# Kernel optimization log

Hardware: AMD Instinct MI355X
Metric: run time of the kernel (lower is better)

The kernel has to match this reference:

```python
import jax, jax.numpy as jnp
import numpy as np

N_HEAD = 16
HEAD_DIM = 64
N_EMBD = N_HEAD * HEAD_DIM
KS, STRIDE = 4, 4
LN_EPS = 1e-5


def _layernorm(x, g, b):
    mu = jnp.mean(x, axis=-1, keepdims=True)
    var = jnp.var(x, axis=-1, keepdims=True)
    return (x - mu) * jax.lax.rsqrt(var + LN_EPS) * g + b


def _depthwise_conv(x_bcl, w):
    # x_bcl: [N, head_dim, L], w: [head_dim, 1, KS] (torch Conv1d groups=head_dim layout)
    return jax.lax.conv_general_dilated(
        x_bcl, w, window_strides=(STRIDE,), padding='VALID',
        dimension_numbers=('NCH', 'OIH', 'NCH'), feature_group_count=HEAD_DIM)


def setup_inputs() -> dict:
    key = jax.random.key(0)
    ks = jax.random.split(key, 12)
    B, T, L = 8, 64, 4096
    s = 0.02
    return {
        'x': jax.random.normal(ks[0], (B, T, N_EMBD), jnp.float32),
        'cached_k': jax.random.normal(ks[1], (B, N_HEAD, L, HEAD_DIM), jnp.float32),
        'cached_v': jax.random.normal(ks[2], (B, N_HEAD, L, HEAD_DIM), jnp.float32),
        'w_attn': jax.random.normal(ks[3], (N_EMBD, 3 * N_EMBD), jnp.float32) * s,
        'b_attn': jnp.zeros((3 * N_EMBD,), jnp.float32),
        'w_proj': jax.random.normal(ks[4], (N_EMBD, N_EMBD), jnp.float32) * s,
        'b_proj': jnp.zeros((N_EMBD,), jnp.float32),
        'k_conv': jax.random.normal(ks[5], (HEAD_DIM, 1, KS), jnp.float32) * 0.5,
        'v_conv': jax.random.normal(ks[6], (HEAD_DIM, 1, KS), jnp.float32) * 0.5,
        'ln_k_g': jnp.ones((HEAD_DIM,), jnp.float32),
        'ln_k_b': jnp.zeros((HEAD_DIM,), jnp.float32),
        'ln_v_g': jnp.ones((HEAD_DIM,), jnp.float32),
        'ln_v_b': jnp.zeros((HEAD_DIM,), jnp.float32),
    }


def reference(x, cached_k, cached_v, w_attn, b_attn, w_proj, b_proj,
              k_conv, v_conv, ln_k_g, ln_k_b, ln_v_g, ln_v_b):
    B, T, C = x.shape
    H, hd = N_HEAD, HEAD_DIM
    qkv = x @ w_attn + b_attn                      # [B,T,3C]
    q, k, v = jnp.split(qkv, 3, axis=-1)
    q = q.reshape(B, T, H, hd).transpose(0, 2, 1, 3)  # [B,H,T,hd]
    k = k.reshape(B, T, H, hd).transpose(0, 2, 1, 3)
    v = v.reshape(B, T, H, hd).transpose(0, 2, 1, 3)

    # compress cached K/V: depthwise conv over cache length, then LayerNorm
    L = cached_k.shape[2]
    pk = cached_k.transpose(0, 1, 3, 2).reshape(B * H, hd, L)
    pv = cached_v.transpose(0, 1, 3, 2).reshape(B * H, hd, L)
    ck = _depthwise_conv(pk, k_conv).reshape(B, H, hd, -1).transpose(0, 1, 3, 2)  # [B,H,Lc,hd]
    cv = _depthwise_conv(pv, v_conv).reshape(B, H, hd, -1).transpose(0, 1, 3, 2)
    ck = jax.lax.stop_gradient(_layernorm(ck, ln_k_g, ln_k_b))
    cv = jax.lax.stop_gradient(_layernorm(cv, ln_v_g, ln_v_b))

    k_full = jnp.concatenate([ck, k], axis=2)      # [B,H,Tk,hd]
    v_full = jnp.concatenate([cv, v], axis=2)
    Tk = k_full.shape[2]

    # faithful to original: rectangular tril(T, Tk) -> query i sees keys j<=i
    mask = jnp.tril(jnp.ones((T, Tk), dtype=bool))
    att = jnp.einsum('bhqd,bhkd->bhqk', q, k_full) * (1.0 / np.sqrt(hd))
    att = jnp.where(mask[None, None], att, -jnp.inf)
    att = jax.nn.softmax(att, axis=-1)
    y = jnp.einsum('bhqk,bhkd->bhqd', att, v_full)
    y = y.transpose(0, 2, 1, 3).reshape(B, T, C)
    return y @ w_proj + b_proj
```

## Files before the change

### kernel.cpp

```cpp
#include <hip/hip_runtime.h>
#include <hip/hip_bf16.h>
#include <math.h>

#define NH 16
#define LCACHE 4096

typedef __attribute__((ext_vector_type(8))) short short8;
typedef __attribute__((ext_vector_type(8))) unsigned short ushort8;
typedef __attribute__((ext_vector_type(4))) float f32x4;

__device__ __forceinline__ unsigned short f2bf(float f) {
    __hip_bfloat16 b = __float2bfloat16(f);
    unsigned short u;
    __builtin_memcpy(&u, &b, 2);
    return u;
}

__global__ __launch_bounds__(256, 4)
void prep_kernel(const float* __restrict__ cached_k, const float* __restrict__ cached_v,
                 const float* __restrict__ kcw, const float* __restrict__ vcw,
                 const float* __restrict__ lkg, const float* __restrict__ lkb,
                 const float* __restrict__ lvg, const float* __restrict__ lvb,
                 const float* __restrict__ x, const float* __restrict__ w_attn,
                 const float* __restrict__ w_proj,
                 ushort* __restrict__ ckf, ushort* __restrict__ cvtf,
                 ushort* __restrict__ xp, ushort* __restrict__ wq,
                 ushort* __restrict__ wp)
{
    __shared__ float Wt[32][65];
    const int bid = blockIdx.x, tid = threadIdx.x;
    const int w = tid >> 6, l = tid & 63;

    const int bh = bid >> 3, sub = bid & 7;
    const int T = sub >> 2, quarter = sub & 3;
    const float* S = (T ? cached_v : cached_k) + (size_t)bh * (LCACHE * 64);
    float tap[4][4];
#pragma unroll
    for (int q = 0; q < 4; ++q) {
        int key = quarter * 16 + w * 4 + q;
        const float* p = S + (size_t)key * 256 + l;
        tap[q][0] = p[0]; tap[q][1] = p[64]; tap[q][2] = p[128]; tap[q][3] = p[192];
    }

    const int isP = bid >> 9;
    const int rem = bid & 511;
    const int ntw = rem >> 5, ktw = (rem >> 1) & 15, kbh = rem & 1;
    const float* W = isP ? w_proj : w_attn;
    const int ldw  = isP ? 1024 : 3072;
    ushort* D      = isP ? wp : wq;
    float wreg[8];
#pragma unroll
    for (int rep = 0; rep < 8; ++rep) {
        int lin = rep * 256 + tid;
        int kr = lin >> 6, nn = lin & 63;
        wreg[rep] = W[(size_t)(ktw * 64 + kbh * 32 + kr) * ldw + ntw * 64 + nn];
    }

    const int doX = (w == (bid & 3));
    float xr[8];
    if (doX) {
        int f = bid;
        int mt = f >> 6, kt = (f >> 2) & 15, fi = f & 3;
        int kb = fi >> 1, mb = fi & 1;
        int r = l & 15, kg8 = l >> 4;
        int m  = mt * 32 + mb * 16 + r;
        int k0 = kt * 64 + kb * 32 + kg8 * 8;
        const float* s = x + (size_t)m * 1024 + k0;
#pragma unroll
        for (int j = 0; j < 8; ++j) xr[j] = s[j];
    }

    {
        const float* cwp = T ? vcw : kcw;
        float4 w4v = *(const float4*)(cwp + l * 4);
        float g = (T ? lvg : lkg)[l], bb = (T ? lvb : lkb)[l];
        ushort* dstf = (T ? cvtf : ckf) + (size_t)bh * 4096;
        float av[4], s1[4], s2[4];
#pragma unroll
        for (int q = 0; q < 4; ++q) {
            float a = tap[q][0] * w4v.x;
            a = fmaf(tap[q][1], w4v.y, a);
            a = fmaf(tap[q][2], w4v.z, a);
            a = fmaf(tap[q][3], w4v.w, a);
            av[q] = a; s1[q] = a; s2[q] = a * a;
        }
#pragma unroll
        for (int o = 32; o; o >>= 1) {
#pragma unroll
            for (int q = 0; q < 4; ++q) {
                s1[q] += __shfl_xor(s1[q], o);
                s2[q] += __shfl_xor(s2[q], o);
            }
        }
#pragma unroll
        for (int q = 0; q < 4; ++q) {
            int key = quarter * 16 + w * 4 + q;
            float mu  = s1[q] * 0.015625f;
            float var = s2[q] * 0.015625f - mu * mu;
            float outv = (av[q] - mu) * rsqrtf(var + 1e-5f) * g + bb;
            unsigned short bf = f2bf(outv);
            const int d = l;
            int off;
            if (T)
                off = ((d >> 4) * 2 + (key >> 5)) * 512
                    + ((key >> 3) & 3) * 128 + (d & 15) * 8 + (key & 7);
            else
                off = ((key >> 4) * 2 + (d >> 5)) * 512
                    + ((d >> 3) & 3) * 128 + (key & 15) * 8 + (d & 7);
            dstf[off] = bf;
        }
    }

    {
#pragma unroll
        for (int rep = 0; rep < 8; ++rep) {
            int lin = rep * 256 + tid;
            Wt[lin >> 6][lin & 63] = wreg[rep];
        }
        __syncthreads();
        int r = l & 15, kg8 = l >> 4;
        ushort8 o;
#pragma unroll
        for (int j = 0; j < 8; ++j)
            o[j] = f2bf(Wt[kg8 * 8 + j][w * 16 + r]);
        size_t f_lin = (size_t)(ntw * 16 + ktw) * 8 + kbh * 4 + w;
        *(ushort8*)(D + f_lin * 512 + l * 8) = o;
    }

    if (doX) {
        ushort8 o;
#pragma unroll
        for (int j = 0; j < 8; ++j) o[j] = f2bf(xr[j]);
        *(ushort8*)(xp + (size_t)bid * 512 + l * 8) = o;
    }
}

__global__ __launch_bounds__(512, 2)
void attn_kernel(const ushort* __restrict__ ckf, const ushort* __restrict__ cvtf,
                 const float* __restrict__ b_attn,
                 const ushort* __restrict__ xp, const ushort* __restrict__ wq,
                 ushort* __restrict__ yp)
{
    __shared__ __align__(16) float qs[32][68];
    __shared__ __align__(16) ushort P_lds[2048];

    const int bid = blockIdx.x;
    const int h    = ((bid & 7) << 1) | ((bid >> 3) & 1);
    const int rem  = bid >> 4;
    const int b    = rem >> 1;
    const int half = rem & 1;
    const int mtA  = b * 2 + half;

    const int tid = threadIdx.x;
    const int w = tid >> 6, l = tid & 63;
    const int kg = w >> 2, w4 = w & 3;
    const int c = l & 15, rg = l >> 4;
    const int g = w & 1, dup = w >> 1;

    const ushort* ckb = ckf + (size_t)(b * NH + h) * 4096;
    const ushort* cvb = cvtf + (size_t)(b * NH + h) * 4096;
    short8 akf[4][2];
#pragma unroll
    for (int mf = 0; mf < 4; ++mf)
#pragma unroll
        for (int kf = 0; kf < 2; ++kf)
            akf[mf][kf] = *(const short8*)(ckb + (mf * 2 + kf) * 512 + l * 8);
    short8 avf[2];
#pragma unroll
    for (int kf = 0; kf < 2; ++kf)
        avf[kf] = *(const short8*)(cvb + (dup * 2 + kf) * 512 + l * 8);

    const ushort* ab = xp + (size_t)mtA * 32768;
    const ushort* bb = wq + (size_t)h * 65536;
    f32x4 acc0 = {0.f,0.f,0.f,0.f}, acc1 = {0.f,0.f,0.f,0.f};
#pragma unroll
    for (int s = 0; s < 8; ++s) {
        const int kt = kg * 8 + s;
        const ushort* A = ab + kt * 2048;
        const ushort* B = bb + kt * 4096;
        short8 a00 = *(const short8*)(A + l * 8);
        short8 a01 = *(const short8*)(A + 512 + l * 8);
        short8 a10 = *(const short8*)(A + 1024 + l * 8);
        short8 a11 = *(const short8*)(A + 1536 + l * 8);
        short8 b0  = *(const short8*)(B + (size_t)w4 * 512 + l * 8);
        short8 b1  = *(const short8*)(B + (size_t)(4 + w4) * 512 + l * 8);
        acc0 = __builtin_amdgcn_mfma_f32_16x16x32_bf16(a00, b0, acc0, 0, 0, 0);
        acc1 = __builtin_amdgcn_mfma_f32_16x16x32_bf16(a01, b0, acc1, 0, 0, 0);
        acc0 = __builtin_amdgcn_mfma_f32_16x16x32_bf16(a10, b1, acc0, 0, 0, 0);
        acc1 = __builtin_amdgcn_mfma_f32_16x16x32_bf16(a11, b1, acc1, 0, 0, 0);
    }

    {
        const int n = w4 * 16 + c;
        if (kg == 0) {
#pragma unroll
            for (int mb = 0; mb < 2; ++mb) {
                f32x4 acc = mb ? acc1 : acc0;
#pragma unroll
                for (int rr = 0; rr < 4; ++rr)
                    qs[mb * 16 + rg * 4 + rr][n] = acc[rr];
            }
        }
        __syncthreads();
        if (kg == 1) {
            float bv = b_attn[h * 64 + n];
#pragma unroll
            for (int mb = 0; mb < 2; ++mb) {
                f32x4 acc = mb ? acc1 : acc0;
#pragma unroll
                for (int rr = 0; rr < 4; ++rr) {
                    int m = mb * 16 + rg * 4 + rr;
                    qs[m][n] = (qs[m][n] + acc[rr] + bv) * 0.125f;
                }
            }
        }
        __syncthreads();
    }

    short8 qb[2];
#pragma unroll
    for (int kf = 0; kf < 2; ++kf) {
        int row = 16 * g + c;
        int d0  = 32 * kf + 8 * rg;
        float4 v0 = *(const float4*)&qs[row][d0];
        float4 v1 = *(const float4*)&qs[row][d0 + 4];
        ushort8 t;
        t[0] = f2bf(v0.x); t[1] = f2bf(v0.y); t[2] = f2bf(v0.z); t[3] = f2bf(v0.w);
        t[4] = f2bf(v1.x); t[5] = f2bf(v1.y); t[6] = f2bf(v1.z); t[7] = f2bf(v1.w);
        qb[kf] = (short8)t;
    }

    f32x4 sacc[4];
#pragma unroll
    for (int mf = 0; mf < 4; ++mf) { sacc[mf][0]=0.f; sacc[mf][1]=0.f; sacc[mf][2]=0.f; sacc[mf][3]=0.f; }
#pragma unroll
    for (int mf = 0; mf < 4; ++mf) {
        sacc[mf] = __builtin_amdgcn_mfma_f32_16x16x32_bf16(akf[mf][0], qb[0], sacc[mf], 0, 0, 0);
        sacc[mf] = __builtin_amdgcn_mfma_f32_16x16x32_bf16(akf[mf][1], qb[1], sacc[mf], 0, 0, 0);
    }

    const int gq = half * 32 + 16 * g + c;
    float pv[4][4];
    float mx = -3.0e38f;
#pragma unroll
    for (int mf = 0; mf < 4; ++mf)
#pragma unroll
        for (int rr = 0; rr < 4; ++rr) {
            int kidx = 16 * mf + 4 * rg + rr;
            float sc = (kidx <= gq) ? sacc[mf][rr] : -3.0e38f;
            pv[mf][rr] = sc;
            mx = fmaxf(mx, sc);
        }
    mx = fmaxf(mx, __shfl_xor(mx, 16));
    mx = fmaxf(mx, __shfl_xor(mx, 32));
    float sum = 0.f;
#pragma unroll
    for (int mf = 0; mf < 4; ++mf)
#pragma unroll
        for (int rr = 0; rr < 4; ++rr) {
            int kidx = 16 * mf + 4 * rg + rr;
            float e = (kidx <= gq) ? __expf(pv[mf][rr] - mx) : 0.f;
            pv[mf][rr] = e;
            sum += e;
        }
    sum += __shfl_xor(sum, 16);
    sum += __shfl_xor(sum, 32);
    float inv = 1.0f / sum;

    if (dup == 0) {
        int q = 16 * g + c;
        int swz = (q & 7) << 3;
#pragma unroll
        for (int mf = 0; mf < 4; ++mf)
#pragma unroll
            for (int rr = 0; rr < 4; ++rr) {
                int kidx = 16 * mf + 4 * rg + rr;
                P_lds[q * 64 + (kidx ^ swz)] = f2bf(pv[mf][rr] * inv);
            }
    }
    __syncthreads();

    short8 pb[2];
#pragma unroll
    for (int kf = 0; kf < 2; ++kf) {
        int q = 16 * g + c;
        int key0 = 32 * kf + 8 * rg;
        pb[kf] = *(const short8*)&P_lds[q * 64 + (key0 ^ ((q & 7) << 3))];
    }
    f32x4 oacc = {0.f, 0.f, 0.f, 0.f};
    oacc = __builtin_amdgcn_mfma_f32_16x16x32_bf16(avf[0], pb[0], oacc, 0, 0, 0);
    oacc = __builtin_amdgcn_mfma_f32_16x16x32_bf16(avf[1], pb[1], oacc, 0, 0, 0);

#pragma unroll
    for (int rr = 0; rr < 4; ++rr) {
        int d  = 16 * dup + 4 * rg + rr;
        int kb = d >> 5, ke = d & 31;
        int l2 = ((ke >> 3) << 4) | c;
        int j2 = ke & 7;
        size_t off = (size_t)mtA * 32768 + (size_t)h * 2048
                   + (size_t)(kb * 2 + g) * 512 + (size_t)l2 * 8 + j2;
        yp[off] = f2bf(oacc[rr]);
    }
}

__global__ __launch_bounds__(512, 2)
void gemm2_kernel(const ushort* __restrict__ Ap, const ushort* __restrict__ Bp,
                  const float* __restrict__ bias, float* __restrict__ C)
{
    __shared__ float red[3][2][32][18];

    const int bid = blockIdx.x;
    const int xcd = bid & 7, idx = bid >> 3;
    const int nt2 = xcd * 4 + (idx & 3);
    const int mt  = idx >> 2;
    const int nt  = nt2 >> 1;
    const int tid = threadIdx.x;
    const int w = tid >> 6, l = tid & 63;
    const int kg = w >> 1, nb2 = w & 1;
    const int nb = (nt2 & 1) * 2 + nb2;
    const int c = l & 15, rg = l >> 4;

    const ushort* ab = Ap + (size_t)mt * 32768;
    const ushort* bb = Bp + (size_t)nt * 65536;
    f32x4 acc0 = {0.f,0.f,0.f,0.f}, acc1 = {0.f,0.f,0.f,0.f};
#pragma unroll
    for (int s = 0; s < 4; ++s) {
        const int kt = kg * 4 + s;
        const ushort* A = ab + kt * 2048;
        const ushort* B = bb + kt * 4096;
        short8 a00 = *(const short8*)(A + l * 8);
        short8 a01 = *(const short8*)(A + 512 + l * 8);
        short8 a10 = *(const short8*)(A + 1024 + l * 8);
        short8 a11 = *(const short8*)(A + 1536 + l * 8);
        short8 b0  = *(const short8*)(B + (size_t)nb * 512 + l * 8);
        short8 b1  = *(const short8*)(B + (size_t)(4 + nb) * 512 + l * 8);
        acc0 = __builtin_amdgcn_mfma_f32_16x16x32_bf16(a00, b0, acc0, 0, 0, 0);
        acc1 = __builtin_amdgcn_mfma_f32_16x16x32_bf16(a01, b0, acc1, 0, 0, 0);
        acc0 = __builtin_amdgcn_mfma_f32_16x16x32_bf16(a10, b1, acc0, 0, 0, 0);
        acc1 = __builtin_amdgcn_mfma_f32_16x16x32_bf16(a11, b1, acc1, 0, 0, 0);
    }

    if (kg > 0) {
#pragma unroll
        for (int mb = 0; mb < 2; ++mb) {
            f32x4 acc = mb ? acc1 : acc0;
#pragma unroll
            for (int rr = 0; rr < 4; ++rr)
                red[kg - 1][nb2][mb * 16 + rg * 4 + rr][c] = acc[rr];
        }
    }
    __syncthreads();
    if (kg == 0) {
        const int n = nt2 * 32 + nb2 * 16 + c;
        float bv = bias[n];
#pragma unroll
        for (int mb = 0; mb < 2; ++mb) {
            f32x4 acc = mb ? acc1 : acc0;
#pragma unroll
            for (int rr = 0; rr < 4; ++rr) {
                int m = mb * 16 + rg * 4 + rr;
                float v = acc[rr] + red[0][nb2][m][c] + red[1][nb2][m][c]
                        + red[2][nb2][m][c] + bv;
                C[(size_t)(mt * 32 + m) * 1024 + n] = v;
            }
        }
    }
}

extern "C" void kernel_launch(void* const* d_in, const int* in_sizes, int n_in,
                              void* d_out, int out_size, void* d_ws, size_t ws_size,
                              hipStream_t stream)
{
    const float* x        = (const float*)d_in[0];
    const float* cached_k = (const float*)d_in[1];
    const float* cached_v = (const float*)d_in[2];
    const float* w_attn   = (const float*)d_in[3];
    const float* b_attn   = (const float*)d_in[4];
    const float* w_proj   = (const float*)d_in[5];
    const float* b_proj   = (const float*)d_in[6];
    const float* k_conv   = (const float*)d_in[7];
    const float* v_conv   = (const float*)d_in[8];
    const float* ln_k_g   = (const float*)d_in[9];
    const float* ln_k_b   = (const float*)d_in[10];
    const float* ln_v_g   = (const float*)d_in[11];
    const float* ln_v_b   = (const float*)d_in[12];

    ushort* xp   = (ushort*)d_ws;
    ushort* wq   = xp + 524288;
    ushort* wp   = wq + 1048576;
    ushort* yp   = wp + 1048576;
    ushort* ckf  = yp + 524288;
    ushort* cvtf = ckf + 524288;
    float* out   = (float*)d_out;

    prep_kernel<<<1024, 256, 0, stream>>>(cached_k, cached_v, k_conv, v_conv,
                                          ln_k_g, ln_k_b, ln_v_g, ln_v_b,
                                          x, w_attn, w_proj, ckf, cvtf, xp, wq, wp);
    attn_kernel<<<256, 512, 0, stream>>>(ckf, cvtf, b_attn, xp, wq, yp);
    gemm2_kernel<<<512, 512, 0, stream>>>(yp, wp, b_proj, out);
}
```

Before: 25.83 us.

## Split attention kernel into 16-query blocks with single softmax wave

The attention kernel now launches 512 blocks of 256 threads, each handling 16 query rows instead of 32. Only one wave per block loads the compressed K fragments and computes scores and softmax, instead of duplicated computation across waves. The goal is more blocks to fill the CUs and less redundant work and register pressure. In exchange the Q-projection GEMM inputs are re-read by more blocks and the other waves idle during softmax.

```diff
diff --git a/kernel.cpp b/kernel.cpp
--- a/kernel.cpp
+++ b/kernel.cpp
@@ -135,157 +135,154 @@
     }
 }
 
-__global__ __launch_bounds__(512, 2)
+__global__ __launch_bounds__(256, 2)
 void attn_kernel(const ushort* __restrict__ ckf, const ushort* __restrict__ cvtf,
                  const float* __restrict__ b_attn,
                  const ushort* __restrict__ xp, const ushort* __restrict__ wq,
                  ushort* __restrict__ yp)
 {
-    __shared__ __align__(16) float qs[32][68];
-    __shared__ __align__(16) ushort P_lds[2048];
+    __shared__ __align__(16) float qs[16][68];
+    __shared__ __align__(16) ushort P_lds[1024];
 
     const int bid = blockIdx.x;
-    const int h    = ((bid & 7) << 1) | ((bid >> 3) & 1);
-    const int rem  = bid >> 4;
-    const int b    = rem >> 1;
-    const int half = rem & 1;
-    const int mtA  = b * 2 + half;
+    const int h   = ((bid & 7) << 1) | ((bid >> 3) & 1);
+    const int rem = bid >> 4;
+    const int b   = rem >> 2;
+    const int q2  = rem & 3;
+    const int mtA = b * 2 + (q2 >> 1);
+    const int mb  = q2 & 1;
 
     const int tid = threadIdx.x;
     const int w = tid >> 6, l = tid & 63;
-    const int kg = w >> 2, w4 = w & 3;
+    const int kg = w >> 1, w2 = w & 1;
     const int c = l & 15, rg = l >> 4;
-    const int g = w & 1, dup = w >> 1;
-
-    const ushort* ckb = ckf + (size_t)(b * NH + h) * 4096;
+    const int qkw = bid & 3;
+
     const ushort* cvb = cvtf + (size_t)(b * NH + h) * 4096;
+    short8 avf[2];
+#pragma unroll
+    for (int kf = 0; kf < 2; ++kf)
+        avf[kf] = *(const short8*)(cvb + (w * 2 + kf) * 512 + l * 8);
+
     short8 akf[4][2];
-#pragma unroll
-    for (int mf = 0; mf < 4; ++mf)
-#pragma unroll
-        for (int kf = 0; kf < 2; ++kf)
-            akf[mf][kf] = *(const short8*)(ckb + (mf * 2 + kf) * 512 + l * 8);
-    short8 avf[2];
-#pragma unroll
-    for (int kf = 0; kf < 2; ++kf)
-        avf[kf] = *(const short8*)(cvb + (dup * 2 + kf) * 512 + l * 8);
-
-    const ushort* ab = xp + (size_t)mtA * 32768;
-    const ushort* bb = wq + (size_t)h * 65536;
+    if (w == qkw) {
+        const ushort* ckb = ckf + (size_t)(b * NH + h) * 4096;
+#pragma unroll
+        for (int mf = 0; mf < 4; ++mf)
+#pragma unroll
+            for (int kf = 0; kf < 2; ++kf)
+                akf[mf][kf] = *(const short8*)(ckb + (mf * 2 + kf) * 512 + l * 8);
+    }
+
+    const ushort* ab = xp + (size_t)mtA * 32768 + mb * 512;
+    const ushort* bb = wq + (size_t)h * 65536 + w2 * 1024;
     f32x4 acc0 = {0.f,0.f,0.f,0.f}, acc1 = {0.f,0.f,0.f,0.f};
 #pragma unroll
     for (int s = 0; s < 8; ++s) {
         const int kt = kg * 8 + s;
         const ushort* A = ab + kt * 2048;
         const ushort* B = bb + kt * 4096;
-        short8 a00 = *(const short8*)(A + l * 8);
-        short8 a01 = *(const short8*)(A + 512 + l * 8);
-        short8 a10 = *(const short8*)(A + 1024 + l * 8);
-        short8 a11 = *(const short8*)(A + 1536 + l * 8);
-        short8 b0  = *(const short8*)(B + (size_t)w4 * 512 + l * 8);
-        short8 b1  = *(const short8*)(B + (size_t)(4 + w4) * 512 + l * 8);
-        acc0 = __builtin_amdgcn_mfma_f32_16x16x32_bf16(a00, b0, acc0, 0, 0, 0);
-        acc1 = __builtin_amdgcn_mfma_f32_16x16x32_bf16(a01, b0, acc1, 0, 0, 0);
-        acc0 = __builtin_amdgcn_mfma_f32_16x16x32_bf16(a10, b1, acc0, 0, 0, 0);
-        acc1 = __builtin_amdgcn_mfma_f32_16x16x32_bf16(a11, b1, acc1, 0, 0, 0);
+        short8 a0  = *(const short8*)(A + l * 8);
+        short8 a1  = *(const short8*)(A + 1024 + l * 8);
+        short8 b00 = *(const short8*)(B + l * 8);
+        short8 b01 = *(const short8*)(B + 512 + l * 8);
+        short8 b10 = *(const short8*)(B + 2048 + l * 8);
+        short8 b11 = *(const short8*)(B + 2560 + l * 8);
+        acc0 = __builtin_amdgcn_mfma_f32_16x16x32_bf16(a0, b00, acc0, 0, 0, 0);
+        acc1 = __builtin_amdgcn_mfma_f32_16x16x32_bf16(a0, b01, acc1, 0, 0, 0);
+        acc0 = __builtin_amdgcn_mfma_f32_16x16x32_bf16(a1, b10, acc0, 0, 0, 0);
+        acc1 = __builtin_amdgcn_mfma_f32_16x16x32_bf16(a1, b11, acc1, 0, 0, 0);
     }
 
     {
-        const int n = w4 * 16 + c;
+        const int n0 = w2 * 32 + c;
         if (kg == 0) {
 #pragma unroll
-            for (int mb = 0; mb < 2; ++mb) {
-                f32x4 acc = mb ? acc1 : acc0;
-#pragma unroll
-                for (int rr = 0; rr < 4; ++rr)
-                    qs[mb * 16 + rg * 4 + rr][n] = acc[rr];
+            for (int rr = 0; rr < 4; ++rr) {
+                qs[rg * 4 + rr][n0]      = acc0[rr];
+                qs[rg * 4 + rr][n0 + 16] = acc1[rr];
             }
         }
         __syncthreads();
         if (kg == 1) {
-            float bv = b_attn[h * 64 + n];
-#pragma unroll
-            for (int mb = 0; mb < 2; ++mb) {
-                f32x4 acc = mb ? acc1 : acc0;
-#pragma unroll
-                for (int rr = 0; rr < 4; ++rr) {
-                    int m = mb * 16 + rg * 4 + rr;
-                    qs[m][n] = (qs[m][n] + acc[rr] + bv) * 0.125f;
-                }
+            float bv0 = b_attn[h * 64 + n0];
+            float bv1 = b_attn[h * 64 + n0 + 16];
+#pragma unroll
+            for (int rr = 0; rr < 4; ++rr) {
+                int m = rg * 4 + rr;
+                qs[m][n0]      = (qs[m][n0]      + acc0[rr] + bv0) * 0.125f;
+                qs[m][n0 + 16] = (qs[m][n0 + 16] + acc1[rr] + bv1) * 0.125f;
             }
         }
         __syncthreads();
     }
 
-    short8 qb[2];
+    if (w == qkw) {
+        short8 qb[2];
+#pragma unroll
+        for (int kf = 0; kf < 2; ++kf) {
+            int d0 = 32 * kf + 8 * rg;
+            float4 v0 = *(const float4*)&qs[c][d0];
+            float4 v1 = *(const float4*)&qs[c][d0 + 4];
+            ushort8 t;
+            t[0] = f2bf(v0.x); t[1] = f2bf(v0.y); t[2] = f2bf(v0.z); t[3] = f2bf(v0.w);
+            t[4] = f2bf(v1.x); t[5] = f2bf(v1.y); t[6] = f2bf(v1.z); t[7] = f2bf(v1.w);
+            qb[kf] = (short8)t;
+        }
+
+        f32x4 sacc[4];
+#pragma unroll
+        for (int mf = 0; mf < 4; ++mf) { sacc[mf][0]=0.f; sacc[mf][1]=0.f; sacc[mf][2]=0.f; sacc[mf][3]=0.f; }
+#pragma unroll
+        for (int mf = 0; mf < 4; ++mf) {
+            sacc[mf] = __builtin_amdgcn_mfma_f32_16x16x32_bf16(akf[mf][0], qb[0], sacc[mf], 0, 0, 0);
+            sacc[mf] = __builtin_amdgcn_mfma_f32_16x16x32_bf16(akf[mf][1], qb[1], sacc[mf], 0, 0, 0);
+        }
+
+        const int gq = q2 * 16 + c;
+        float pv[4][4];
+        float mx = -3.0e38f;
+#pragma unroll
+        for (int mf = 0; mf < 4; ++mf)
+#pragma unroll
+            for (int rr = 0; rr < 4; ++rr) {
+                int kidx = 16 * mf + 4 * rg + rr;
+                float sc = (kidx <= gq) ? sacc[mf][rr] : -3.0e38f;
+                pv[mf][rr] = sc;
+                mx = fmaxf(mx, sc);
+            }
+        mx = fmaxf(mx, __shfl_xor(mx, 16));
+        mx = fmaxf(mx, __shfl_xor(mx, 32));
+        float sum = 0.f;
+#pragma unroll
+        for (int mf = 0; mf < 4; ++mf)
+#pragma unroll
+            for (int rr = 0; rr < 4; ++rr) {
+                int kidx = 16 * mf + 4 * rg + rr;
+                float e = (kidx <= gq) ? __expf(pv[mf][rr] - mx) : 0.f;
+                pv[mf][rr] = e;
+                sum += e;
+            }
+        sum += __shfl_xor(sum, 16);
+        sum += __shfl_xor(sum, 32);
+        float inv = 1.0f / sum;
+
+        int swz = (c & 7) << 3;
+#pragma unroll
+        for (int mf = 0; mf < 4; ++mf)
+#pragma unroll
+            for (int rr = 0; rr < 4; ++rr) {
+                int kidx = 16 * mf + 4 * rg + rr;
+                P_lds[c * 64 + (kidx ^ swz)] = f2bf(pv[mf][rr] * inv);
+            }
+    }
+    __syncthreads();
+
+    short8 pb[2];
 #pragma unroll
     for (int kf = 0; kf < 2; ++kf) {
-        int row = 16 * g + c;
-        int d0  = 32 * kf + 8 * rg;
-        float4 v0 = *(const float4*)&qs[row][d0];
-        float4 v1 = *(const float4*)&qs[row][d0 + 4];
-        ushort8 t;
-        t[0] = f2bf(v0.x); t[1] = f2bf(v0.y); t[2] = f2bf(v0.z); t[3] = f2bf(v0.w);
-        t[4] = f2bf(v1.x); t[5] = f2bf(v1.y); t[6] = f2bf(v1.z); t[7] = f2bf(v1.w);
-        qb[kf] = (short8)t;
-    }
-
-    f32x4 sacc[4];
-#pragma unroll
-    for (int mf = 0; mf < 4; ++mf) { sacc[mf][0]=0.f; sacc[mf][1]=0.f; sacc[mf][2]=0.f; sacc[mf][3]=0.f; }
-#pragma unroll
-    for (int mf = 0; mf < 4; ++mf) {
-        sacc[mf] = __builtin_amdgcn_mfma_f32_16x16x32_bf16(akf[mf][0], qb[0], sacc[mf], 0, 0, 0);
-        sacc[mf] = __builtin_amdgcn_mfma_f32_16x16x32_bf16(akf[mf][1], qb[1], sacc[mf], 0, 0, 0);
-    }
-
-    const int gq = half * 32 + 16 * g + c;
-    float pv[4][4];
-    float mx = -3.0e38f;
-#pragma unroll
-    for (int mf = 0; mf < 4; ++mf)
-#pragma unroll
-        for (int rr = 0; rr < 4; ++rr) {
-            int kidx = 16 * mf + 4 * rg + rr;
-            float sc = (kidx <= gq) ? sacc[mf][rr] : -3.0e38f;
-            pv[mf][rr] = sc;
-            mx = fmaxf(mx, sc);
-        }
-    mx = fmaxf(mx, __shfl_xor(mx, 16));
-    mx = fmaxf(mx, __shfl_xor(mx, 32));
-    float sum = 0.f;
-#pragma unroll
-    for (int mf = 0; mf < 4; ++mf)
-#pragma unroll
-        for (int rr = 0; rr < 4; ++rr) {
-            int kidx = 16 * mf + 4 * rg + rr;
-            float e = (kidx <= gq) ? __expf(pv[mf][rr] - mx) : 0.f;
-            pv[mf][rr] = e;
-            sum += e;
-        }
-    sum += __shfl_xor(sum, 16);
-    sum += __shfl_xor(sum, 32);
-    float inv = 1.0f / sum;
-
-    if (dup == 0) {
-        int q = 16 * g + c;
-        int swz = (q & 7) << 3;
-#pragma unroll
-        for (int mf = 0; mf < 4; ++mf)
-#pragma unroll
-            for (int rr = 0; rr < 4; ++rr) {
-                int kidx = 16 * mf + 4 * rg + rr;
-                P_lds[q * 64 + (kidx ^ swz)] = f2bf(pv[mf][rr] * inv);
-            }
-    }
-    __syncthreads();
-
-    short8 pb[2];
-#pragma unroll
-    for (int kf = 0; kf < 2; ++kf) {
-        int q = 16 * g + c;
         int key0 = 32 * kf + 8 * rg;
-        pb[kf] = *(const short8*)&P_lds[q * 64 + (key0 ^ ((q & 7) << 3))];
+        pb[kf] = *(const short8*)&P_lds[c * 64 + (key0 ^ ((c & 7) << 3))];
     }
     f32x4 oacc = {0.f, 0.f, 0.f, 0.f};
     oacc = __builtin_amdgcn_mfma_f32_16x16x32_bf16(avf[0], pb[0], oacc, 0, 0, 0);
@@ -293,12 +290,12 @@
 
 #pragma unroll
     for (int rr = 0; rr < 4; ++rr) {
-        int d  = 16 * dup + 4 * rg + rr;
+        int d  = 16 * w + 4 * rg + rr;
         int kb = d >> 5, ke = d & 31;
         int l2 = ((ke >> 3) << 4) | c;
         int j2 = ke & 7;
         size_t off = (size_t)mtA * 32768 + (size_t)h * 2048
-                   + (size_t)(kb * 2 + g) * 512 + (size_t)l2 * 8 + j2;
+                   + (size_t)(kb * 2 + mb) * 512 + (size_t)l2 * 8 + j2;
         yp[off] = f2bf(oacc[rr]);
     }
 }
@@ -396,6 +393,6 @@
     prep_kernel<<<1024, 256, 0, stream>>>(cached_k, cached_v, k_conv, v_conv,
                                           ln_k_g, ln_k_b, ln_v_g, ln_v_b,
                                           x, w_attn, w_proj, ckf, cvtf, xp, wq, wp);
-    attn_kernel<<<256, 512, 0, stream>>>(ckf, cvtf, b_attn, xp, wq, yp);
+    attn_kernel<<<512, 256, 0, stream>>>(ckf, cvtf, b_attn, xp, wq, yp);
     gemm2_kernel<<<512, 512, 0, stream>>>(yp, wp, b_proj, out);
 }
```

After: 25.83 us, median of 2. About the same (-0.0%).
